# Optimization experiments

Measured on AMD Instinct MI355X. Metric: run time of the kernel, lower is better.

Reference implementation:

```python
import jax, jax.numpy as jnp
import numpy as np

N = 50000
E = 800000
IN_DIM = 128
HID = 32
HEADS = 4
OUT_DIM = 32
NEG_SLOPE = 0.2


def setup_inputs() -> dict:
    key = jax.random.key(0)
    ks = jax.random.split(key, 10)
    x = jax.random.normal(ks[0], (N, IN_DIM), dtype=jnp.float32)
    edge_index = jax.random.randint(ks[1], (2, E), 0, N, dtype=jnp.int64)
    # layer 1: in 128 -> 4 heads x 32, concat
    W1 = jax.random.normal(ks[2], (IN_DIM, HEADS * HID), dtype=jnp.float32) * (1.0 / np.sqrt(IN_DIM))
    a_src1 = jax.random.normal(ks[3], (HEADS, HID), dtype=jnp.float32) * 0.1
    a_dst1 = jax.random.normal(ks[4], (HEADS, HID), dtype=jnp.float32) * 0.1
    b1 = jnp.zeros((HEADS * HID,), dtype=jnp.float32)
    # layer 2: in 128 -> 1 head x 32, mean
    W2 = jax.random.normal(ks[5], (HEADS * HID, OUT_DIM), dtype=jnp.float32) * (1.0 / np.sqrt(HEADS * HID))
    a_src2 = jax.random.normal(ks[6], (1, OUT_DIM), dtype=jnp.float32) * 0.1
    a_dst2 = jax.random.normal(ks[7], (1, OUT_DIM), dtype=jnp.float32) * 0.1
    b2 = jnp.zeros((OUT_DIM,), dtype=jnp.float32)
    return {"x": x, "edge_index": edge_index, "W1": W1, "a_src1": a_src1,
            "a_dst1": a_dst1, "b1": b1, "W2": W2, "a_src2": a_src2,
            "a_dst2": a_dst2, "b2": b2}


def gat_layer(x, src, dst, W, a_src, a_dst, b, heads, concat, num_nodes):
    # linear transform -> [N, H, C]
    h = (x @ W).reshape(num_nodes, heads, -1)
    # per-node attention halves, gathered per edge -> [E, H]
    alpha = jax.nn.leaky_relu((h * a_src).sum(-1)[src] + (h * a_dst).sum(-1)[dst],
                              negative_slope=NEG_SLOPE)
    # segment softmax over edges grouped by destination node
    seg_max = jax.ops.segment_max(alpha, dst, num_segments=num_nodes)
    e = jnp.exp(alpha - seg_max[dst])
    denom = jax.ops.segment_sum(e, dst, num_segments=num_nodes)[dst]
    w = e / jnp.maximum(denom, 1e-16)
    # weighted message scatter-sum -> [N, H, C]
    out = jax.ops.segment_sum(h[src] * w[..., None], dst, num_segments=num_nodes)
    out = out.reshape(num_nodes, -1) if concat else out.mean(axis=1)
    return out + b


def reference(x, edge_index, W1, a_src1, a_dst1, b1, W2, a_src2, a_dst2, b2):
    num_nodes = x.shape[0]
    loops = jnp.arange(num_nodes, dtype=edge_index.dtype)
    src = jnp.concatenate([edge_index[0], loops])  # add self-loops (PyG default)
    dst = jnp.concatenate([edge_index[1], loops])
    h = jax.nn.relu(gat_layer(x, src, dst, W1, a_src1, a_dst1, b1, HEADS, True, num_nodes))
    out = gat_layer(h, src, dst, W2, a_src2, a_dst2, b2, 1, False, num_nodes)
    return jax.nn.sigmoid(out)
```

## Files before the change

kernel.cpp:

```cpp
#include <hip/hip_runtime.h>
#include <math.h>

#define NN 50000
#define NE 800000
#define NT (NN + NE)
#define SCAN_BLOCKS 196

__device__ __forceinline__ float lrelu(float a) { return a > 0.f ? a : 0.2f * a; }

__device__ __forceinline__ float sel4(float4 v, int h) {
  float r = v.x;
  r = (h == 1) ? v.y : r;
  r = (h == 2) ? v.z : r;
  r = (h == 3) ? v.w : r;
  return r;
}

__device__ __forceinline__ unsigned int f2bf(float f) {
  unsigned int u = __float_as_uint(f);
  return (u + 0x7FFFu + ((u >> 16) & 1u)) >> 16;
}
__device__ __forceinline__ unsigned int packbf(float lo, float hi) {
  return f2bf(lo) | (f2bf(hi) << 16);
}
__device__ __forceinline__ float bflo(unsigned int v) { return __uint_as_float(v << 16); }
__device__ __forceinline__ float bfhi(unsigned int v) { return __uint_as_float(v & 0xFFFF0000u); }

__global__ void k_detect(const unsigned int* __restrict__ eb, int* __restrict__ flag) {
  __shared__ int nz;
  if (threadIdx.x == 0) nz = 0;
  __syncthreads();
  int local = 0;
  for (int i = threadIdx.x; i < 2048; i += 256) local |= (eb[2 * i + 1] != 0u);
  if (local) nz = 1;
  __syncthreads();
  if (threadIdx.x == 0) *flag = (nz == 0) ? 1 : 0;
}

__global__ __launch_bounds__(256) void k_pass1(const void* __restrict__ eb,
                                               const int* __restrict__ flag,
                                               int* __restrict__ cnt,
                                               unsigned int* __restrict__ pw) {
  int e0 = (blockIdx.x * 256 + threadIdx.x) * 4;
  if (e0 >= NT) return;
  int is64 = *flag;
  int d0, d1, d2, d3;
  if (e0 < NE) {
    if (is64) {
      const uint4* p = (const uint4*)((const unsigned int*)eb + 2 * ((size_t)NE + e0));
      uint4 a = p[0], b = p[1];
      d0 = (int)a.x; d1 = (int)a.z; d2 = (int)b.x; d3 = (int)b.z;
    } else {
      int4 v = *(const int4*)((const int*)eb + (size_t)NE + e0);
      d0 = v.x; d1 = v.y; d2 = v.z; d3 = v.w;
    }
  } else {
    d0 = e0 - NE; d1 = d0 + 1; d2 = d0 + 2; d3 = d0 + 3;
  }
  unsigned int p0 = (unsigned int)atomicAdd(&cnt[d0], 1);
  unsigned int p1 = (unsigned int)atomicAdd(&cnt[d1], 1);
  unsigned int p2 = (unsigned int)atomicAdd(&cnt[d2], 1);
  unsigned int p3 = (unsigned int)atomicAdd(&cnt[d3], 1);
  *(uint4*)&pw[e0] = make_uint4(p0, p1, p2, p3);
}

__global__ __launch_bounds__(256) void k_bsum(const int* __restrict__ cnt,
                                              int* __restrict__ bsum) {
  int i = blockIdx.x * 256 + threadIdx.x;
  int v = (i < NN) ? cnt[i] : 0;
#pragma unroll
  for (int off = 1; off < 64; off <<= 1) v += __shfl_xor(v, off, 64);
  __shared__ int ws[4];
  int lane = threadIdx.x & 63, wid = threadIdx.x >> 6;
  if (lane == 0) ws[wid] = v;
  __syncthreads();
  if (threadIdx.x == 0) bsum[blockIdx.x] = ws[0] + ws[1] + ws[2] + ws[3];
}

__global__ __launch_bounds__(256) void k_bscan(const int* __restrict__ bsum,
                                               int* __restrict__ boff,
                                               int* __restrict__ rowp) {
  int t = threadIdx.x;
  int lane = t & 63, wid = t >> 6;
  int v = (t < SCAN_BLOCKS) ? bsum[t] : 0;
  int incl = v;
#pragma unroll
  for (int off = 1; off < 64; off <<= 1) {
    int u = __shfl_up(incl, off, 64);
    if (lane >= off) incl += u;
  }
  __shared__ int wsum[4], woff[4];
  if (lane == 63) wsum[wid] = incl;
  __syncthreads();
  if (t == 0) {
    woff[0] = 0;
    woff[1] = wsum[0];
    woff[2] = wsum[0] + wsum[1];
    woff[3] = wsum[0] + wsum[1] + wsum[2];
  }
  __syncthreads();
  if (t < SCAN_BLOCKS) boff[t] = woff[wid] + incl - v;
  if (t == 0) rowp[NN] = NT;
}

__global__ __launch_bounds__(256) void k_rowp(const int* __restrict__ cnt,
                                              const int* __restrict__ boff,
                                              int* __restrict__ rowp) {
  int i = blockIdx.x * 256 + threadIdx.x;
  int t = threadIdx.x;
  int lane = t & 63, wid = t >> 6;
  int v = (i < NN) ? cnt[i] : 0;
  int incl = v;
#pragma unroll
  for (int off = 1; off < 64; off <<= 1) {
    int u = __shfl_up(incl, off, 64);
    if (lane >= off) incl += u;
  }
  __shared__ int wsum[4], woff[4];
  if (lane == 63) wsum[wid] = incl;
  __syncthreads();
  if (t == 0) {
    woff[0] = 0;
    woff[1] = wsum[0];
    woff[2] = wsum[0] + wsum[1];
    woff[3] = wsum[0] + wsum[1] + wsum[2];
  }
  __syncthreads();
  if (i < NN) rowp[i] = boff[blockIdx.x] + woff[wid] + incl - v;
}

__global__ __launch_bounds__(256) void k_pass2(const void* __restrict__ eb,
                                               const int* __restrict__ flag,
                                               const int* __restrict__ rowp,
                                               const unsigned int* __restrict__ pw,
                                               int* __restrict__ csr) {
  int e0 = (blockIdx.x * 256 + threadIdx.x) * 4;
  if (e0 >= NT) return;
  int is64 = *flag;
  int s0, s1, s2, s3, d0, d1, d2, d3;
  if (e0 < NE) {
    if (is64) {
      const uint4* ps = (const uint4*)((const unsigned int*)eb + 2 * (size_t)e0);
      uint4 a = ps[0], b = ps[1];
      s0 = (int)a.x; s1 = (int)a.z; s2 = (int)b.x; s3 = (int)b.z;
      const uint4* pd = (const uint4*)((const unsigned int*)eb + 2 * ((size_t)NE + e0));
      uint4 c = pd[0], d = pd[1];
      d0 = (int)c.x; d1 = (int)c.z; d2 = (int)d.x; d3 = (int)d.z;
    } else {
      int4 vs = *(const int4*)((const int*)eb + (size_t)e0);
      s0 = vs.x; s1 = vs.y; s2 = vs.z; s3 = vs.w;
      int4 vd = *(const int4*)((const int*)eb + (size_t)NE + e0);
      d0 = vd.x; d1 = vd.y; d2 = vd.z; d3 = vd.w;
    }
  } else {
    s0 = d0 = e0 - NE;
    s1 = d1 = d0 + 1;
    s2 = d2 = d0 + 2;
    s3 = d3 = d0 + 3;
  }
  uint4 pv = *(const uint4*)&pw[e0];
  csr[rowp[d0] + (int)pv.x] = s0;
  csr[rowp[d1] + (int)pv.y] = s1;
  csr[rowp[d2] + (int)pv.z] = s2;
  csr[rowp[d3] + (int)pv.w] = s3;
}

__global__ __launch_bounds__(256) void k_gemm1(const float* __restrict__ X,
                                               const float* __restrict__ W,
                                               const float* __restrict__ a_src,
                                               const float* __restrict__ a_dst,
                                               uint4* __restrict__ Hb,
                                               float* __restrict__ AS,
                                               float* __restrict__ AD) {
  __shared__ float xs[64][36];
  __shared__ float ws[32][132];
  int tid = threadIdx.x;
  int tx = tid & 15, ty = tid >> 4;
  int r0 = blockIdx.x * 64;
  float acc[4][8];
#pragma unroll
  for (int i = 0; i < 4; ++i)
#pragma unroll
    for (int j = 0; j < 8; ++j) acc[i][j] = 0.f;

  for (int kb = 0; kb < 4; ++kb) {
    __syncthreads();
#pragma unroll
    for (int i = tid; i < 512; i += 256) {
      int row = i >> 3, c4 = i & 7;
      int gr = r0 + row;
      float4 v = make_float4(0.f, 0.f, 0.f, 0.f);
      if (gr < NN) v = ((const float4*)X)[(size_t)gr * 32 + kb * 8 + c4];
      *(float4*)&xs[row][c4 * 4] = v;
    }
#pragma unroll
    for (int i = tid; i < 1024; i += 256) {
      int kr = i >> 5, c4 = i & 31;
      *(float4*)&ws[kr][c4 * 4] = ((const float4*)W)[(size_t)(kb * 32 + kr) * 32 + c4];
    }
    __syncthreads();
#pragma unroll 4
    for (int k = 0; k < 32; ++k) {
      float xr[4];
#pragma unroll
      for (int i = 0; i < 4; ++i) xr[i] = xs[ty * 4 + i][k];
      float4 w0 = *(const float4*)&ws[k][tx * 8];
      float4 w1 = *(const float4*)&ws[k][tx * 8 + 4];
#pragma unroll
      for (int i = 0; i < 4; ++i) {
        acc[i][0] += xr[i] * w0.x;
        acc[i][1] += xr[i] * w0.y;
        acc[i][2] += xr[i] * w0.z;
        acc[i][3] += xr[i] * w0.w;
        acc[i][4] += xr[i] * w1.x;
        acc[i][5] += xr[i] * w1.y;
        acc[i][6] += xr[i] * w1.z;
        acc[i][7] += xr[i] * w1.w;
      }
    }
  }
  float4 s0 = ((const float4*)a_src)[tx * 2];
  float4 s1 = ((const float4*)a_src)[tx * 2 + 1];
  float4 d0 = ((const float4*)a_dst)[tx * 2];
  float4 d1 = ((const float4*)a_dst)[tx * 2 + 1];
  int head = tx >> 2;
#pragma unroll
  for (int i = 0; i < 4; ++i) {
    int gr = r0 + ty * 4 + i;
    float ps = acc[i][0] * s0.x + acc[i][1] * s0.y + acc[i][2] * s0.z + acc[i][3] * s0.w +
               acc[i][4] * s1.x + acc[i][5] * s1.y + acc[i][6] * s1.z + acc[i][7] * s1.w;
    float pd = acc[i][0] * d0.x + acc[i][1] * d0.y + acc[i][2] * d0.z + acc[i][3] * d0.w +
               acc[i][4] * d1.x + acc[i][5] * d1.y + acc[i][6] * d1.z + acc[i][7] * d1.w;
    ps += __shfl_xor(ps, 1, 64);
    ps += __shfl_xor(ps, 2, 64);
    pd += __shfl_xor(pd, 1, 64);
    pd += __shfl_xor(pd, 2, 64);
    if (gr < NN) {
      Hb[(size_t)gr * 16 + tx] =
          make_uint4(packbf(acc[i][0], acc[i][1]), packbf(acc[i][2], acc[i][3]),
                     packbf(acc[i][4], acc[i][5]), packbf(acc[i][6], acc[i][7]));
      if ((tx & 3) == 0) {
        AS[gr * 4 + head] = ps;
        AD[gr * 4 + head] = pd;
      }
    }
  }
}

__global__ __launch_bounds__(256) void k_l1node(const int* __restrict__ rowp,
                                                const int* __restrict__ csr,
                                                const uint4* __restrict__ Hb,
                                                const float* __restrict__ AS,
                                                const float* __restrict__ AD,
                                                const float* __restrict__ b1,
                                                float* __restrict__ HM) {
  int lane = threadIdx.x & 63, wid = threadIdx.x >> 6;
  int n = blockIdx.x * 4 + wid;
  if (n >= NN) return;
  int beg = rowp[n], end = rowp[n + 1];
  float4 ad4 = *(const float4*)&AD[n * 4];

  int sl = lane & 15;
  int g = lane >> 4;
  int hd = sl >> 2;
  float adh = sel4(ad4, hd);

  float a0 = 0.f, a1 = 0.f, a2 = 0.f, a3 = 0.f, a4 = 0.f, a5 = 0.f, a6 = 0.f, a7 = 0.f;
  float esum = 0.f;
  int i = beg + g;
  for (; i + 4 < end; i += 8) {
    int sA = csr[i];
    int sB = csr[i + 4];
    float lA = AS[sA * 4 + hd];
    float lB = AS[sB * 4 + hd];
    uint4 hA = Hb[(size_t)sA * 16 + sl];
    uint4 hB = Hb[(size_t)sB * 16 + sl];
    float wA = __expf(lrelu(lA + adh));
    float wB = __expf(lrelu(lB + adh));
    esum += wA + wB;
    a0 += wA * bflo(hA.x) + wB * bflo(hB.x);
    a1 += wA * bfhi(hA.x) + wB * bfhi(hB.x);
    a2 += wA * bflo(hA.y) + wB * bflo(hB.y);
    a3 += wA * bfhi(hA.y) + wB * bfhi(hB.y);
    a4 += wA * bflo(hA.z) + wB * bflo(hB.z);
    a5 += wA * bfhi(hA.z) + wB * bfhi(hB.z);
    a6 += wA * bflo(hA.w) + wB * bflo(hB.w);
    a7 += wA * bfhi(hA.w) + wB * bfhi(hB.w);
  }
  if (i < end) {
    int s = csr[i];
    float l = AS[s * 4 + hd];
    uint4 hv = Hb[(size_t)s * 16 + sl];
    float w0 = __expf(lrelu(l + adh));
    esum += w0;
    a0 += w0 * bflo(hv.x);
    a1 += w0 * bfhi(hv.x);
    a2 += w0 * bflo(hv.y);
    a3 += w0 * bfhi(hv.y);
    a4 += w0 * bflo(hv.z);
    a5 += w0 * bfhi(hv.z);
    a6 += w0 * bflo(hv.w);
    a7 += w0 * bfhi(hv.w);
  }
#pragma unroll
  for (int off = 16; off < 64; off <<= 1) {
    esum += __shfl_xor(esum, off, 64);
    a0 += __shfl_xor(a0, off, 64);
    a1 += __shfl_xor(a1, off, 64);
    a2 += __shfl_xor(a2, off, 64);
    a3 += __shfl_xor(a3, off, 64);
    a4 += __shfl_xor(a4, off, 64);
    a5 += __shfl_xor(a5, off, 64);
    a6 += __shfl_xor(a6, off, 64);
    a7 += __shfl_xor(a7, off, 64);
  }
  if (lane < 16) {
    float r = 1.f / esum;
    int c = sl * 8;
    float4 bva = *(const float4*)&b1[c];
    float4 bvb = *(const float4*)&b1[c + 4];
    *(float4*)&HM[(size_t)n * 128 + c] =
        make_float4(fmaxf(a0 * r + bva.x, 0.f), fmaxf(a1 * r + bva.y, 0.f),
                    fmaxf(a2 * r + bva.z, 0.f), fmaxf(a3 * r + bva.w, 0.f));
    *(float4*)&HM[(size_t)n * 128 + c + 4] =
        make_float4(fmaxf(a4 * r + bvb.x, 0.f), fmaxf(a5 * r + bvb.y, 0.f),
                    fmaxf(a6 * r + bvb.z, 0.f), fmaxf(a7 * r + bvb.w, 0.f));
  }
}

__global__ __launch_bounds__(256) void k_gemm2(const float* __restrict__ HM,
                                               const float* __restrict__ W2,
                                               const float* __restrict__ a_src2,
                                               const float* __restrict__ a_dst2,
                                               uint4* __restrict__ Hb2,
                                               float* __restrict__ AS,
                                               float* __restrict__ AD) {
  __shared__ float wsm[128 * 32];
  __shared__ float xs[256][33];
  int tid = threadIdx.x;
  for (int i = tid; i < 1024; i += 256) ((float4*)wsm)[i] = ((const float4*)W2)[i];
  int r = blockIdx.x * 256 + tid;
  float acc[32];
#pragma unroll
  for (int j = 0; j < 32; ++j) acc[j] = 0.f;

  for (int kb = 0; kb < 4; ++kb) {
    __syncthreads();
#pragma unroll
    for (int i = tid; i < 2048; i += 256) {
      int row = i >> 3, c4 = i & 7;
      int gr = blockIdx.x * 256 + row;
      float4 v = make_float4(0.f, 0.f, 0.f, 0.f);
      if (gr < NN) v = ((const float4*)HM)[(size_t)gr * 32 + kb * 8 + c4];
      float* p = &xs[row][c4 * 4];
      p[0] = v.x; p[1] = v.y; p[2] = v.z; p[3] = v.w;
    }
    __syncthreads();
#pragma unroll 4
    for (int k = 0; k < 32; ++k) {
      float xv = xs[tid][k];
      const float4* wr = (const float4*)&wsm[(kb * 32 + k) * 32];
#pragma unroll
      for (int j4 = 0; j4 < 8; ++j4) {
        float4 wv = wr[j4];
        acc[j4 * 4 + 0] += xv * wv.x;
        acc[j4 * 4 + 1] += xv * wv.y;
        acc[j4 * 4 + 2] += xv * wv.z;
        acc[j4 * 4 + 3] += xv * wv.w;
      }
    }
  }
  if (r < NN) {
    float ps = 0.f, pd = 0.f;
    unsigned int pk[16];
#pragma unroll
    for (int j4 = 0; j4 < 8; ++j4) {
      float4 sv = ((const float4*)a_src2)[j4];
      float4 dv = ((const float4*)a_dst2)[j4];
      ps += acc[j4 * 4 + 0] * sv.x + acc[j4 * 4 + 1] * sv.y +
            acc[j4 * 4 + 2] * sv.z + acc[j4 * 4 + 3] * sv.w;
      pd += acc[j4 * 4 + 0] * dv.x + acc[j4 * 4 + 1] * dv.y +
            acc[j4 * 4 + 2] * dv.z + acc[j4 * 4 + 3] * dv.w;
      pk[j4 * 2]     = packbf(acc[j4 * 4 + 0], acc[j4 * 4 + 1]);
      pk[j4 * 2 + 1] = packbf(acc[j4 * 4 + 2], acc[j4 * 4 + 3]);
    }
#pragma unroll
    for (int q = 0; q < 4; ++q)
      Hb2[(size_t)r * 4 + q] =
          make_uint4(pk[q * 4], pk[q * 4 + 1], pk[q * 4 + 2], pk[q * 4 + 3]);
    AS[r] = ps;
    AD[r] = pd;
  }
}

__global__ __launch_bounds__(256) void k_l2node(const int* __restrict__ rowp,
                                                const int* __restrict__ csr,
                                                const uint2* __restrict__ Hb2,
                                                const float* __restrict__ AS,
                                                const float* __restrict__ AD,
                                                const float* __restrict__ b2,
                                                float* __restrict__ out) {
  int lane = threadIdx.x & 63, wid = threadIdx.x >> 6;
  int n = blockIdx.x * 4 + wid;
  if (n >= NN) return;
  int beg = rowp[n], end = rowp[n + 1];
  float adn = AD[n];

  int sl = lane & 7;
  int g = lane >> 3;
  float a0 = 0.f, a1 = 0.f, a2 = 0.f, a3 = 0.f;
  float esum = 0.f;
  int i = beg + g;
  for (; i + 8 < end; i += 16) {
    int sA = csr[i];
    int sB = csr[i + 8];
    float lA = AS[sA];
    float lB = AS[sB];
    uint2 hA = Hb2[(size_t)sA * 8 + sl];
    uint2 hB = Hb2[(size_t)sB * 8 + sl];
    float wA = __expf(lrelu(lA + adn));
    float wB = __expf(lrelu(lB + adn));
    esum += wA + wB;
    a0 += wA * bflo(hA.x) + wB * bflo(hB.x);
    a1 += wA * bfhi(hA.x) + wB * bfhi(hB.x);
    a2 += wA * bflo(hA.y) + wB * bflo(hB.y);
    a3 += wA * bfhi(hA.y) + wB * bfhi(hB.y);
  }
  if (i < end) {
    int s = csr[i];
    float l = AS[s];
    uint2 hv = Hb2[(size_t)s * 8 + sl];
    float w0 = __expf(lrelu(l + adn));
    esum += w0;
    a0 += w0 * bflo(hv.x);
    a1 += w0 * bfhi(hv.x);
    a2 += w0 * bflo(hv.y);
    a3 += w0 * bfhi(hv.y);
  }
#pragma unroll
  for (int off = 8; off < 64; off <<= 1) {
    esum += __shfl_xor(esum, off, 64);
    a0 += __shfl_xor(a0, off, 64);
    a1 += __shfl_xor(a1, off, 64);
    a2 += __shfl_xor(a2, off, 64);
    a3 += __shfl_xor(a3, off, 64);
  }
  if (lane < 8) {
    float r = 1.f / esum;
    int c = sl * 4;
    float4 bv = *(const float4*)&b2[c];
    float vx = a0 * r + bv.x, vy = a1 * r + bv.y, vz = a2 * r + bv.z, vw = a3 * r + bv.w;
    *(float4*)&out[(size_t)n * 32 + c] =
        make_float4(1.f / (1.f + __expf(-vx)), 1.f / (1.f + __expf(-vy)),
                    1.f / (1.f + __expf(-vz)), 1.f / (1.f + __expf(-vw)));
  }
}

extern "C" void kernel_launch(void* const* d_in, const int* in_sizes, int n_in,
                              void* d_out, int out_size, void* d_ws, size_t ws_size,
                              hipStream_t stream) {
  (void)in_sizes; (void)n_in; (void)out_size; (void)ws_size;
  const float* x      = (const float*)d_in[0];
  const void*  eb     = d_in[1];
  const float* W1     = (const float*)d_in[2];
  const float* a_src1 = (const float*)d_in[3];
  const float* a_dst1 = (const float*)d_in[4];
  const float* b1     = (const float*)d_in[5];
  const float* W2     = (const float*)d_in[6];
  const float* a_src2 = (const float*)d_in[7];
  const float* a_dst2 = (const float*)d_in[8];
  const float* b2     = (const float*)d_in[9];
  float* out = (float*)d_out;

  char* w = (char*)d_ws;
  auto alloc = [&](size_t bytes) {
    char* p = w;
    w += (bytes + 255) & ~(size_t)255;
    return p;
  };
  int*          flag = (int*)alloc(4);
  int*          cnt  = (int*)alloc((size_t)NN * 4);
  int*          rowp = (int*)alloc((size_t)(NN + 1) * 4);
  unsigned int* pw   = (unsigned int*)alloc((size_t)NT * 4);
  int*          csr  = (int*)alloc((size_t)NT * 4);
  int*          bsum = (int*)alloc((size_t)SCAN_BLOCKS * 4);
  int*          boff = (int*)alloc((size_t)SCAN_BLOCKS * 4);
  uint4*        Hb1  = (uint4*)alloc((size_t)NN * 128 * 2);
  float*        AS1  = (float*)alloc((size_t)NN * 16);
  float*        AD1  = (float*)alloc((size_t)NN * 16);
  float*        HM   = (float*)alloc((size_t)NN * 128 * 4);
  uint4* Hb2 = Hb1;
  float* AS2 = (float*)cnt;
  float* AD2 = (float*)pw;

  hipMemsetAsync(cnt, 0, (size_t)NN * 4, stream);
  k_detect<<<1, 256, 0, stream>>>((const unsigned int*)eb, flag);
  int egrid4 = (NT / 4 + 255) / 256;
  k_pass1<<<egrid4, 256, 0, stream>>>(eb, flag, cnt, pw);
  k_bsum<<<SCAN_BLOCKS, 256, 0, stream>>>(cnt, bsum);
  k_bscan<<<1, 256, 0, stream>>>(bsum, boff, rowp);
  k_rowp<<<SCAN_BLOCKS, 256, 0, stream>>>(cnt, boff, rowp);
  k_pass2<<<egrid4, 256, 0, stream>>>(eb, flag, rowp, pw, csr);

  k_gemm1<<<(NN + 63) / 64, 256, 0, stream>>>(x, W1, a_src1, a_dst1, Hb1, AS1, AD1);
  k_l1node<<<(NN + 3) / 4, 256, 0, stream>>>(rowp, csr, Hb1, AS1, AD1, b1, HM);
  k_gemm2<<<(NN + 255) / 256, 256, 0, stream>>>(HM, W2, a_src2, a_dst2, Hb2, AS2, AD2);
  k_l2node<<<(NN + 3) / 4, 256, 0, stream>>>(rowp, csr, (const uint2*)Hb2, AS2, AD2, b2, out);
}
```

Baseline: 282.3 us.

## Store layer-1 output as bf16 and split gemm2 K across four lanes

```diff
diff --git a/kernel.cpp b/kernel.cpp
--- a/kernel.cpp
+++ b/kernel.cpp
@@ -253,7 +253,7 @@
                                                 const float* __restrict__ AS,
                                                 const float* __restrict__ AD,
                                                 const float* __restrict__ b1,
-                                                float* __restrict__ HM) {
+                                                uint4* __restrict__ HMb) {
   int lane = threadIdx.x & 63, wid = threadIdx.x >> 6;
   int n = blockIdx.x * 4 + wid;
   if (n >= NN) return;
@@ -319,16 +319,20 @@
     int c = sl * 8;
     float4 bva = *(const float4*)&b1[c];
     float4 bvb = *(const float4*)&b1[c + 4];
-    *(float4*)&HM[(size_t)n * 128 + c] =
-        make_float4(fmaxf(a0 * r + bva.x, 0.f), fmaxf(a1 * r + bva.y, 0.f),
-                    fmaxf(a2 * r + bva.z, 0.f), fmaxf(a3 * r + bva.w, 0.f));
-    *(float4*)&HM[(size_t)n * 128 + c + 4] =
-        make_float4(fmaxf(a4 * r + bvb.x, 0.f), fmaxf(a5 * r + bvb.y, 0.f),
-                    fmaxf(a6 * r + bvb.z, 0.f), fmaxf(a7 * r + bvb.w, 0.f));
-  }
-}
-
-__global__ __launch_bounds__(256) void k_gemm2(const float* __restrict__ HM,
+    float v0 = fmaxf(a0 * r + bva.x, 0.f);
+    float v1 = fmaxf(a1 * r + bva.y, 0.f);
+    float v2 = fmaxf(a2 * r + bva.z, 0.f);
+    float v3 = fmaxf(a3 * r + bva.w, 0.f);
+    float v4 = fmaxf(a4 * r + bvb.x, 0.f);
+    float v5 = fmaxf(a5 * r + bvb.y, 0.f);
+    float v6 = fmaxf(a6 * r + bvb.z, 0.f);
+    float v7 = fmaxf(a7 * r + bvb.w, 0.f);
+    HMb[(size_t)n * 16 + sl] =
+        make_uint4(packbf(v0, v1), packbf(v2, v3), packbf(v4, v5), packbf(v6, v7));
+  }
+}
+
+__global__ __launch_bounds__(256) void k_gemm2(const uint4* __restrict__ HMb,
                                                const float* __restrict__ W2,
                                                const float* __restrict__ a_src2,
                                                const float* __restrict__ a_dst2,
@@ -336,60 +340,66 @@
                                                float* __restrict__ AS,
                                                float* __restrict__ AD) {
   __shared__ float wsm[128 * 32];
-  __shared__ float xs[256][33];
   int tid = threadIdx.x;
   for (int i = tid; i < 1024; i += 256) ((float4*)wsm)[i] = ((const float4*)W2)[i];
-  int r = blockIdx.x * 256 + tid;
+  __syncthreads();
+  int rl = tid >> 2, sub = tid & 3;
+  int r = blockIdx.x * 64 + rl;
   float acc[32];
 #pragma unroll
   for (int j = 0; j < 32; ++j) acc[j] = 0.f;
 
-  for (int kb = 0; kb < 4; ++kb) {
-    __syncthreads();
-#pragma unroll
-    for (int i = tid; i < 2048; i += 256) {
-      int row = i >> 3, c4 = i & 7;
-      int gr = blockIdx.x * 256 + row;
-      float4 v = make_float4(0.f, 0.f, 0.f, 0.f);
-      if (gr < NN) v = ((const float4*)HM)[(size_t)gr * 32 + kb * 8 + c4];
-      float* p = &xs[row][c4 * 4];
-      p[0] = v.x; p[1] = v.y; p[2] = v.z; p[3] = v.w;
-    }
-    __syncthreads();
-#pragma unroll 4
-    for (int k = 0; k < 32; ++k) {
-      float xv = xs[tid][k];
-      const float4* wr = (const float4*)&wsm[(kb * 32 + k) * 32];
+  if (r < NN) {
+    const uint4* xp = &HMb[(size_t)r * 16 + sub * 4];
+    uint4 xq0 = xp[0], xq1 = xp[1], xq2 = xp[2], xq3 = xp[3];
+    int kbase = sub * 32;
+    unsigned int wds[16] = {xq0.x, xq0.y, xq0.z, xq0.w, xq1.x, xq1.y, xq1.z, xq1.w,
+                            xq2.x, xq2.y, xq2.z, xq2.w, xq3.x, xq3.y, xq3.z, xq3.w};
+#pragma unroll
+    for (int t = 0; t < 16; ++t) {
+      float xlo = bflo(wds[t]);
+      float xhi = bfhi(wds[t]);
+      const float4* wr0 = (const float4*)&wsm[(kbase + t * 2) * 32];
+      const float4* wr1 = (const float4*)&wsm[(kbase + t * 2 + 1) * 32];
 #pragma unroll
       for (int j4 = 0; j4 < 8; ++j4) {
-        float4 wv = wr[j4];
-        acc[j4 * 4 + 0] += xv * wv.x;
-        acc[j4 * 4 + 1] += xv * wv.y;
-        acc[j4 * 4 + 2] += xv * wv.z;
-        acc[j4 * 4 + 3] += xv * wv.w;
+        float4 w0 = wr0[j4];
+        float4 w1 = wr1[j4];
+        acc[j4 * 4 + 0] += xlo * w0.x + xhi * w1.x;
+        acc[j4 * 4 + 1] += xlo * w0.y + xhi * w1.y;
+        acc[j4 * 4 + 2] += xlo * w0.z + xhi * w1.z;
+        acc[j4 * 4 + 3] += xlo * w0.w + xhi * w1.w;
       }
     }
   }
+#pragma unroll
+  for (int j = 0; j < 32; ++j) {
+    acc[j] += __shfl_xor(acc[j], 1, 64);
+    acc[j] += __shfl_xor(acc[j], 2, 64);
+  }
   if (r < NN) {
-    float ps = 0.f, pd = 0.f;
-    unsigned int pk[16];
-#pragma unroll
-    for (int j4 = 0; j4 < 8; ++j4) {
-      float4 sv = ((const float4*)a_src2)[j4];
-      float4 dv = ((const float4*)a_dst2)[j4];
-      ps += acc[j4 * 4 + 0] * sv.x + acc[j4 * 4 + 1] * sv.y +
-            acc[j4 * 4 + 2] * sv.z + acc[j4 * 4 + 3] * sv.w;
-      pd += acc[j4 * 4 + 0] * dv.x + acc[j4 * 4 + 1] * dv.y +
-            acc[j4 * 4 + 2] * dv.z + acc[j4 * 4 + 3] * dv.w;
-      pk[j4 * 2]     = packbf(acc[j4 * 4 + 0], acc[j4 * 4 + 1]);
-      pk[j4 * 2 + 1] = packbf(acc[j4 * 4 + 2], acc[j4 * 4 + 3]);
-    }
-#pragma unroll
-    for (int q = 0; q < 4; ++q)
-      Hb2[(size_t)r * 4 + q] =
-          make_uint4(pk[q * 4], pk[q * 4 + 1], pk[q * 4 + 2], pk[q * 4 + 3]);
-    AS[r] = ps;
-    AD[r] = pd;
+    int c = sub * 8;
+    float4 sv0 = ((const float4*)a_src2)[sub * 2];
+    float4 sv1 = ((const float4*)a_src2)[sub * 2 + 1];
+    float4 dv0 = ((const float4*)a_dst2)[sub * 2];
+    float4 dv1 = ((const float4*)a_dst2)[sub * 2 + 1];
+    float ps = acc[c + 0] * sv0.x + acc[c + 1] * sv0.y + acc[c + 2] * sv0.z +
+               acc[c + 3] * sv0.w + acc[c + 4] * sv1.x + acc[c + 5] * sv1.y +
+               acc[c + 6] * sv1.z + acc[c + 7] * sv1.w;
+    float pd = acc[c + 0] * dv0.x + acc[c + 1] * dv0.y + acc[c + 2] * dv0.z +
+               acc[c + 3] * dv0.w + acc[c + 4] * dv1.x + acc[c + 5] * dv1.y +
+               acc[c + 6] * dv1.z + acc[c + 7] * dv1.w;
+    ps += __shfl_xor(ps, 1, 64);
+    ps += __shfl_xor(ps, 2, 64);
+    pd += __shfl_xor(pd, 1, 64);
+    pd += __shfl_xor(pd, 2, 64);
+    Hb2[(size_t)r * 4 + sub] =
+        make_uint4(packbf(acc[c + 0], acc[c + 1]), packbf(acc[c + 2], acc[c + 3]),
+                   packbf(acc[c + 4], acc[c + 5]), packbf(acc[c + 6], acc[c + 7]));
+    if (sub == 0) {
+      AS[r] = ps;
+      AD[r] = pd;
+    }
   }
 }
 
@@ -488,7 +498,7 @@
   uint4*        Hb1  = (uint4*)alloc((size_t)NN * 128 * 2);
   float*        AS1  = (float*)alloc((size_t)NN * 16);
   float*        AD1  = (float*)alloc((size_t)NN * 16);
-  float*        HM   = (float*)alloc((size_t)NN * 128 * 4);
+  uint4*        HMb  = (uint4*)alloc((size_t)NN * 128 * 2);
   uint4* Hb2 = Hb1;
   float* AS2 = (float*)cnt;
   float* AD2 = (float*)pw;
@@ -503,7 +513,7 @@
   k_pass2<<<egrid4, 256, 0, stream>>>(eb, flag, rowp, pw, csr);
 
   k_gemm1<<<(NN + 63) / 64, 256, 0, stream>>>(x, W1, a_src1, a_dst1, Hb1, AS1, AD1);
-  k_l1node<<<(NN + 3) / 4, 256, 0, stream>>>(rowp, csr, Hb1, AS1, AD1, b1, HM);
-  k_gemm2<<<(NN + 255) / 256, 256, 0, stream>>>(HM, W2, a_src2, a_dst2, Hb2, AS2, AD2);
+  k_l1node<<<(NN + 3) / 4, 256, 0, stream>>>(rowp, csr, Hb1, AS1, AD1, b1, HMb);
+  k_gemm2<<<(NN + 63) / 64, 256, 0, stream>>>(HMb, W2, a_src2, a_dst2, Hb2, AS2, AD2);
   k_l2node<<<(NN + 3) / 4, 256, 0, stream>>>(rowp, csr, (const uint2*)Hb2, AS2, AD2, b2, out);
 }
```

After: 275.5 us. 2.4% less time.
